# Kernel tuning notes

Hardware: AMD Instinct MI355X
Metric: run time of the kernel (lower is better)

## Reference

```python
import jax, jax.numpy as jnp
import numpy as np

S = 7          # grid_size
B = 2          # num_boxes
C = 80         # num_classes
LC = 5.0       # lambda_coord
LN = 0.5       # lambda_noobj
BT = 8192      # batch
N = 32         # gt boxes per image (distinct cells)


def setup_inputs() -> dict:
    key = jax.random.key(0)
    kp, kc, ko, kw, kl = jax.random.split(key, 5)
    preds = jax.random.normal(kp, (BT, S, S, B * 5 + C), jnp.float32)
    # choose N distinct grid cells per image so scatter-set is deterministic
    cells = jnp.argsort(jax.random.uniform(kc, (BT, S * S)), axis=-1)[:, :N]
    gi = cells % S
    gj = cells // S
    off = jax.random.uniform(ko, (BT, N, 2), minval=0.05, maxval=0.95)
    cx = (gi.astype(jnp.float32) + off[..., 0]) / S
    cy = (gj.astype(jnp.float32) + off[..., 1]) / S
    wh = jax.random.uniform(kw, (BT, N, 2), minval=0.05, maxval=0.3)
    gt_boxes = jnp.stack([cx - 0.5 * wh[..., 0], cy - 0.5 * wh[..., 1],
                          cx + 0.5 * wh[..., 0], cy + 0.5 * wh[..., 1]], axis=-1)
    gt_labels = jax.random.randint(kl, (BT, N), 0, C)
    gt_valid = jnp.ones((BT, N), dtype=bool)
    return {"preds": preds, "gt_boxes": gt_boxes,
            "gt_labels": gt_labels, "gt_valid": gt_valid}


def reference(preds, gt_boxes, gt_labels, gt_valid):
    Bt = preds.shape[0]
    dt = preds.dtype
    pred_cls = preds[..., B * 5:]                              # [Bt,S,S,C]
    pb = preds[..., :B * 5].reshape(Bt, S, S, B, 5)            # [Bt,S,S,B,5]

    x1, y1, x2, y2 = (gt_boxes[..., i] for i in range(4))      # each [Bt,N]
    cx = (x1 + x2) * 0.5
    cy = (y1 + y2) * 0.5
    w = jnp.maximum(x2 - x1, 1e-6)
    h = jnp.maximum(y2 - y1, 1e-6)
    gi = jnp.clip(jnp.floor(cx * S), 0, S - 1).astype(jnp.int32)
    gj = jnp.clip(jnp.floor(cy * S), 0, S - 1).astype(jnp.int32)

    bidx = jnp.arange(Bt, dtype=jnp.int32)[:, None]
    cell = pb[bidx, gj, gi]                                    # [Bt,N,B,5]

    # decode predicted boxes for the matched cell
    px = (jax.nn.sigmoid(cell[..., 0]) + gi[..., None].astype(dt)) / S
    py = (jax.nn.sigmoid(cell[..., 1]) + gj[..., None].astype(dt)) / S
    pw = cell[..., 2] ** 2
    ph = cell[..., 3] ** 2
    px1 = px - 0.5 * pw; py1 = py - 0.5 * ph
    px2 = px + 0.5 * pw; py2 = py + 0.5 * ph

    # IoU of B predicted boxes vs the gt box, vectorized over [Bt,N]
    gx1 = x1[..., None]; gy1 = y1[..., None]
    gx2 = x2[..., None]; gy2 = y2[..., None]
    iw = jnp.clip(jnp.minimum(px2, gx2) - jnp.maximum(px1, gx1), 0.0)
    ih = jnp.clip(jnp.minimum(py2, gy2) - jnp.maximum(py1, gy1), 0.0)
    inter = iw * ih
    area_p = (px2 - px1) * (py2 - py1)
    area_g = ((x2 - x1) * (y2 - y1))[..., None]
    ious = inter / (area_p + area_g - inter + 1e-6)            # [Bt,N,B]

    best = jnp.argmax(ious, axis=-1)                           # [Bt,N]
    iou_best = jax.lax.stop_gradient(
        jnp.take_along_axis(ious, best[..., None], axis=-1)[..., 0])

    # scatter target assignment (distinct cells -> deterministic set)
    flat_pb = Bt * S * S * B
    idx = ((bidx * S + gj) * S + gi) * B + best.astype(jnp.int32)
    idx = jnp.where(gt_valid, idx, flat_pb)                    # OOB -> dropped
    obj = jnp.zeros(flat_pb, bool).at[idx].set(True, mode='drop').reshape(Bt, S, S, B)
    conf_t = jnp.zeros(flat_pb, dt).at[idx].set(iou_best, mode='drop').reshape(Bt, S, S, B)
    tgt = jnp.stack([cx * S - gi.astype(dt), cy * S - gj.astype(dt),
                     jnp.sqrt(w), jnp.sqrt(h)], axis=-1)       # [Bt,N,4]
    coord_t = jnp.zeros((flat_pb, 4), dt).at[idx].set(tgt, mode='drop').reshape(Bt, S, S, B, 4)
    flat_c = Bt * S * S * C
    cidx = ((bidx * S + gj) * S + gi) * C + gt_labels.astype(jnp.int32)
    cidx = jnp.where(gt_valid, cidx, flat_c)
    cls_t = jnp.zeros(flat_c, dt).at[cidx].set(1.0, mode='drop').reshape(Bt, S, S, C)

    # masked MSE reductions
    pm = obj.astype(dt)
    nm = 1.0 - pm
    cm = obj.any(axis=-1).astype(dt)
    n_pos = jnp.maximum(pm.sum(), 1.0)
    n_neg = jnp.maximum(nm.sum(), 1.0)
    n_cell = jnp.maximum(cm.sum(), 1.0)

    sx = jax.nn.sigmoid(pb[..., 0])
    sy = jax.nn.sigmoid(pb[..., 1])
    so = jax.nn.sigmoid(pb[..., 4])
    loss_x = (pm * (sx - coord_t[..., 0]) ** 2).sum()
    loss_y = (pm * (sy - coord_t[..., 1]) ** 2).sum()
    loss_w = (pm * (pb[..., 2] - coord_t[..., 2]) ** 2).sum()
    loss_h = (pm * (pb[..., 3] - coord_t[..., 3]) ** 2).sum()
    loss_coord = LC * (loss_x + loss_y + loss_w + loss_h) / n_pos
    loss_obj = (pm * (so - conf_t) ** 2).sum() / n_pos
    loss_noobj = LN * (nm * (so - conf_t) ** 2).sum() / n_neg
    sp = jax.nn.softmax(pred_cls, axis=-1)
    loss_cls = (cm * ((sp - cls_t) ** 2).sum(axis=-1)).sum() / n_cell
    return loss_coord + loss_obj + loss_noobj + loss_cls
```

## Files before the change

### kernel.cpp

```cpp
#include <hip/hip_runtime.h>

#define S7 7
#define NCH 90
#define NCELL 49
#define NGT 32
#define IMG_FLOATS (NCELL * NCH)
#define IMG_F2     (IMG_FLOATS / 2)

__device__ __forceinline__ float sigm(float x) { return 1.0f / (1.0f + __expf(-x)); }

__global__ __launch_bounds__(256) void yolo_fused(
    const float*  __restrict__ preds,
    const float4* __restrict__ gt_boxes,
    const int*    __restrict__ gt_labels,
    float* __restrict__ ws,
    float c_coord, float c_obj, float c_noobj, float c_cls)
{
    __shared__ float s_img[IMG_FLOATS];
    __shared__ float s_red[4];

    const int t = threadIdx.x;
    const int b = blockIdx.x;
    const int g = t >> 3, u = t & 7;

    const int n = b * NGT + g;
    float4 gb = gt_boxes[n];
    int lab = gt_labels[n];

    const float2* img2 = (const float2*)(preds + (size_t)b * IMG_FLOATS);
    float2* s2 = (float2*)s_img;
    float2 v[9];
    #pragma unroll
    for (int k = 0; k < 9; ++k) {
        int idx = t + k * 256;
        if (idx < IMG_F2) v[k] = img2[idx];
    }
    #pragma unroll
    for (int k = 0; k < 9; ++k) {
        int idx = t + k * 256;
        if (idx < IMG_F2) s2[idx] = v[k];
    }

    float x1 = gb.x, y1 = gb.y, x2 = gb.z, y2 = gb.w;
    float cx = (x1 + x2) * 0.5f, cy = (y1 + y2) * 0.5f;
    float gif = fminf(fmaxf(floorf(cx * 7.f), 0.f), 6.f);
    float gjf = fminf(fmaxf(floorf(cy * 7.f), 0.f), 6.f);
    int cell = (int)gjf * S7 + (int)gif;

    __syncthreads();

    float part = 0.f;

    if (t < 2 * NCELL) {
        float so = sigm(s_img[(t >> 1) * NCH + 4 + 5 * (t & 1)]);
        part += c_noobj * so * so;
    }

    const float2* row2 = s2 + cell * (NCH / 2);
    float s = 0.f, q = 0.f, el = 0.f;
    {
        #pragma unroll
        for (int k = 0; k < 5; ++k) {
            float2 cv = row2[5 + 5 * u + k];
            float e0 = __expf(cv.x);
            float e1 = __expf(cv.y);
            int cid = 10 * u + 2 * k;
            s += e0 + e1;
            q = fmaf(e0, e0, q);
            q = fmaf(e1, e1, q);
            el = (cid     == lab) ? e0 : el;
            el = (cid + 1 == lab) ? e1 : el;
        }
        #pragma unroll
        for (int off = 1; off <= 4; off <<= 1) {
            s  += __shfl_xor(s,  off, 64);
            q  += __shfl_xor(q,  off, 64);
            el += __shfl_xor(el, off, 64);
        }
    }

    if (u == 0) {
        float inv = 1.f / s;
        part += c_cls * fmaf(q * inv, inv, fmaf(-2.f * el, inv, 1.f));

        float2 b0 = row2[0], b1 = row2[1], b2 = row2[2], b3 = row2[3], b4 = row2[4];
        float c[10] = {b0.x, b0.y, b1.x, b1.y, b2.x, b2.y, b3.x, b3.y, b4.x, b4.y};
        float w = fmaxf(x2 - x1, 1e-6f), h = fmaxf(y2 - y1, 1e-6f);
        float ag = (x2 - x1) * (y2 - y1);
        const float inv7 = 0.14285714285714285f;
        float iou[2];
        #pragma unroll
        for (int bb = 0; bb < 2; ++bb) {
            float px = (sigm(c[bb * 5 + 0]) + gif) * inv7;
            float py = (sigm(c[bb * 5 + 1]) + gjf) * inv7;
            float pw = c[bb * 5 + 2] * c[bb * 5 + 2];
            float ph = c[bb * 5 + 3] * c[bb * 5 + 3];
            float px1 = px - 0.5f * pw, px2 = px + 0.5f * pw;
            float py1 = py - 0.5f * ph, py2 = py + 0.5f * ph;
            float iw = fmaxf(fminf(px2, x2) - fmaxf(px1, x1), 0.f);
            float ih = fmaxf(fminf(py2, y2) - fmaxf(py1, y1), 0.f);
            float inter = iw * ih;
            float ap = (px2 - px1) * (py2 - py1);
            iou[bb] = inter / (ap + ag - inter + 1e-6f);
        }
        int best = (iou[1] > iou[0]) ? 1 : 0;
        float ioub = iou[best];
        float soB  = sigm(c[best * 5 + 4]);
        part += c_obj * (soB - ioub) * (soB - ioub);
        part -= c_noobj * soB * soB;
        float tx = cx * 7.f - gif, ty = cy * 7.f - gjf;
        float sx = sigm(c[best * 5 + 0]), sy = sigm(c[best * 5 + 1]);
        float dx = sx - tx, dy = sy - ty;
        float dw = c[best * 5 + 2] - sqrtf(w), dh = c[best * 5 + 3] - sqrtf(h);
        part += c_coord * (dx * dx + dy * dy + dw * dw + dh * dh);
    }

    #pragma unroll
    for (int off = 32; off >= 1; off >>= 1) part += __shfl_xor(part, off, 64);
    if ((t & 63) == 0) s_red[t >> 6] = part;
    __syncthreads();
    if (t == 0) ws[b] = s_red[0] + s_red[1] + s_red[2] + s_red[3];
}

__global__ __launch_bounds__(256) void yolo_reduce(const float* __restrict__ ws,
                                                   float* __restrict__ out, int n) {
    float v = 0.f;
    for (int i = threadIdx.x; i < n; i += 256) v += ws[i];
    #pragma unroll
    for (int off = 32; off >= 1; off >>= 1) v += __shfl_xor(v, off, 64);
    __shared__ float r[4];
    if ((threadIdx.x & 63) == 0) r[threadIdx.x >> 6] = v;
    __syncthreads();
    if (threadIdx.x == 0) out[0] = r[0] + r[1] + r[2] + r[3];
}

extern "C" void kernel_launch(void* const* d_in, const int* in_sizes, int n_in,
                              void* d_out, int out_size, void* d_ws, size_t ws_size,
                              hipStream_t stream)
{
    const float*  preds     = (const float*)d_in[0];
    const float4* gt_boxes  = (const float4*)d_in[1];
    const int*    gt_labels = (const int*)d_in[2];
    int Bt = in_sizes[0] / IMG_FLOATS;

    float n_pos = (float)Bt * NGT;
    float n_neg = (float)Bt * (2 * NCELL - NGT);
    float c_coord = 5.0f / n_pos;
    float c_obj   = 1.0f / n_pos;
    float c_noobj = 0.5f / n_neg;
    float c_cls   = 1.0f / n_pos;

    float* ws = (float*)d_ws;
    yolo_fused<<<dim3(Bt), dim3(256), 0, stream>>>(preds, gt_boxes, gt_labels, ws,
                                                   c_coord, c_obj, c_noobj, c_cls);
    yolo_reduce<<<dim3(1), dim3(256), 0, stream>>>(ws, (float*)d_out, Bt);
}
```

Baseline: 218.2 us.

## Make fused YOLO loss kernel persistent with double-buffered LDS prefetch

Launches at most 2048 blocks that loop over images in grid-stride order. The next image's predictions and gt data are loaded into registers while the current image is processed from one of two LDS buffers. This aims to hide global load latency and cut per-block launch and sync overhead, and the final reduction now covers fewer partials. The doubled LDS footprint and extra registers lower occupancy, which can offset the overlap.

```diff
diff --git a/kernel.cpp b/kernel.cpp
--- a/kernel.cpp
+++ b/kernel.cpp
@@ -6,6 +6,8 @@
 #define NGT 32
 #define IMG_FLOATS (NCELL * NCH)
 #define IMG_F2     (IMG_FLOATS / 2)
+#define LDS_F2     2208
+#define MAXBLK 2048
 
 __device__ __forceinline__ float sigm(float x) { return 1.0f / (1.0f + __expf(-x)); }
 
@@ -14,112 +16,129 @@
     const float4* __restrict__ gt_boxes,
     const int*    __restrict__ gt_labels,
     float* __restrict__ ws,
-    float c_coord, float c_obj, float c_noobj, float c_cls)
+    float c_coord, float c_obj, float c_noobj, float c_cls, int Bt)
 {
-    __shared__ float s_img[IMG_FLOATS];
-    __shared__ float s_red[4];
+    __shared__ float2 s_buf[2][LDS_F2];
+    __shared__ float  s_red[4];
 
     const int t = threadIdx.x;
-    const int b = blockIdx.x;
     const int g = t >> 3, u = t & 7;
+    const float inv7 = 0.14285714285714285f;
 
-    const int n = b * NGT + g;
-    float4 gb = gt_boxes[n];
-    int lab = gt_labels[n];
+    float part = 0.f;
+    int b = blockIdx.x;
+    int p = 0;
 
-    const float2* img2 = (const float2*)(preds + (size_t)b * IMG_FLOATS);
-    float2* s2 = (float2*)s_img;
-    float2 v[9];
-    #pragma unroll
-    for (int k = 0; k < 9; ++k) {
-        int idx = t + k * 256;
-        if (idx < IMG_F2) v[k] = img2[idx];
+    {
+        const float2* img2 = (const float2*)(preds + (size_t)b * IMG_FLOATS);
+        float2 v[9];
+        #pragma unroll
+        for (int k = 0; k < 9; ++k) { int i = t + k * 256; if (i < IMG_F2) v[k] = img2[i]; }
+        #pragma unroll
+        for (int k = 0; k < 9; ++k) { int i = t + k * 256; if (i < IMG_F2) s_buf[0][i] = v[k]; }
     }
-    #pragma unroll
-    for (int k = 0; k < 9; ++k) {
-        int idx = t + k * 256;
-        if (idx < IMG_F2) s2[idx] = v[k];
-    }
-
-    float x1 = gb.x, y1 = gb.y, x2 = gb.z, y2 = gb.w;
-    float cx = (x1 + x2) * 0.5f, cy = (y1 + y2) * 0.5f;
-    float gif = fminf(fmaxf(floorf(cx * 7.f), 0.f), 6.f);
-    float gjf = fminf(fmaxf(floorf(cy * 7.f), 0.f), 6.f);
-    int cell = (int)gjf * S7 + (int)gif;
-
+    float4 gb = gt_boxes[b * NGT + g];
+    int   lab = gt_labels[b * NGT + g];
     __syncthreads();
 
-    float part = 0.f;
+    while (true) {
+        const int bn = b + gridDim.x;
+        const bool more = bn < Bt;
 
-    if (t < 2 * NCELL) {
-        float so = sigm(s_img[(t >> 1) * NCH + 4 + 5 * (t & 1)]);
-        part += c_noobj * so * so;
-    }
+        float2 nv[9];
+        float4 ngb; int nlab;
+        if (more) {
+            const float2* img2 = (const float2*)(preds + (size_t)bn * IMG_FLOATS);
+            #pragma unroll
+            for (int k = 0; k < 9; ++k) { int i = t + k * 256; if (i < IMG_F2) nv[k] = img2[i]; }
+            ngb  = gt_boxes[bn * NGT + g];
+            nlab = gt_labels[bn * NGT + g];
+        }
 
-    const float2* row2 = s2 + cell * (NCH / 2);
-    float s = 0.f, q = 0.f, el = 0.f;
-    {
+        const float*  buff = (const float*)s_buf[p];
+        {
+            if (t < 2 * NCELL) {
+                float so = sigm(buff[(t >> 1) * NCH + 4 + 5 * (t & 1)]);
+                part += c_noobj * so * so;
+            }
+
+            float x1 = gb.x, y1 = gb.y, x2 = gb.z, y2 = gb.w;
+            float cx = (x1 + x2) * 0.5f, cy = (y1 + y2) * 0.5f;
+            float gif = fminf(fmaxf(floorf(cx * 7.f), 0.f), 6.f);
+            float gjf = fminf(fmaxf(floorf(cy * 7.f), 0.f), 6.f);
+            int cell = (int)gjf * S7 + (int)gif;
+            const float2* row2 = s_buf[p] + cell * (NCH / 2);
+
+            float s = 0.f, q = 0.f, el = 0.f;
+            #pragma unroll
+            for (int k = 0; k < 5; ++k) {
+                float2 cv = row2[5 + 5 * u + k];
+                float e0 = __expf(cv.x);
+                float e1 = __expf(cv.y);
+                int cid = 10 * u + 2 * k;
+                s += e0 + e1;
+                q = fmaf(e0, e0, q);
+                q = fmaf(e1, e1, q);
+                el = (cid     == lab) ? e0 : el;
+                el = (cid + 1 == lab) ? e1 : el;
+            }
+            #pragma unroll
+            for (int off = 1; off <= 4; off <<= 1) {
+                s  += __shfl_xor(s,  off, 64);
+                q  += __shfl_xor(q,  off, 64);
+                el += __shfl_xor(el, off, 64);
+            }
+
+            if (u == 0) {
+                float inv = 1.f / s;
+                part += c_cls * fmaf(q * inv, inv, fmaf(-2.f * el, inv, 1.f));
+
+                float2 b0 = row2[0], b1 = row2[1], b2 = row2[2], b3 = row2[3], b4 = row2[4];
+                float c[10] = {b0.x, b0.y, b1.x, b1.y, b2.x, b2.y, b3.x, b3.y, b4.x, b4.y};
+                float w = fmaxf(x2 - x1, 1e-6f), h = fmaxf(y2 - y1, 1e-6f);
+                float ag = (x2 - x1) * (y2 - y1);
+                float iou[2];
+                #pragma unroll
+                for (int bb = 0; bb < 2; ++bb) {
+                    float px = (sigm(c[bb * 5 + 0]) + gif) * inv7;
+                    float py = (sigm(c[bb * 5 + 1]) + gjf) * inv7;
+                    float pw = c[bb * 5 + 2] * c[bb * 5 + 2];
+                    float ph = c[bb * 5 + 3] * c[bb * 5 + 3];
+                    float px1 = px - 0.5f * pw, px2 = px + 0.5f * pw;
+                    float py1 = py - 0.5f * ph, py2 = py + 0.5f * ph;
+                    float iw = fmaxf(fminf(px2, x2) - fmaxf(px1, x1), 0.f);
+                    float ih = fmaxf(fminf(py2, y2) - fmaxf(py1, y1), 0.f);
+                    float inter = iw * ih;
+                    float ap = (px2 - px1) * (py2 - py1);
+                    iou[bb] = inter / (ap + ag - inter + 1e-6f);
+                }
+                int best = (iou[1] > iou[0]) ? 1 : 0;
+                float ioub = iou[best];
+                float soB  = sigm(c[best * 5 + 4]);
+                part += c_obj * (soB - ioub) * (soB - ioub);
+                part -= c_noobj * soB * soB;
+                float tx = cx * 7.f - gif, ty = cy * 7.f - gjf;
+                float sx = sigm(c[best * 5 + 0]), sy = sigm(c[best * 5 + 1]);
+                float dx = sx - tx, dy = sy - ty;
+                float dw = c[best * 5 + 2] - sqrtf(w), dh = c[best * 5 + 3] - sqrtf(h);
+                part += c_coord * (dx * dx + dy * dy + dw * dw + dh * dh);
+            }
+        }
+
+        if (!more) break;
+
         #pragma unroll
-        for (int k = 0; k < 5; ++k) {
-            float2 cv = row2[5 + 5 * u + k];
-            float e0 = __expf(cv.x);
-            float e1 = __expf(cv.y);
-            int cid = 10 * u + 2 * k;
-            s += e0 + e1;
-            q = fmaf(e0, e0, q);
-            q = fmaf(e1, e1, q);
-            el = (cid     == lab) ? e0 : el;
-            el = (cid + 1 == lab) ? e1 : el;
-        }
-        #pragma unroll
-        for (int off = 1; off <= 4; off <<= 1) {
-            s  += __shfl_xor(s,  off, 64);
-            q  += __shfl_xor(q,  off, 64);
-            el += __shfl_xor(el, off, 64);
-        }
-    }
-
-    if (u == 0) {
-        float inv = 1.f / s;
-        part += c_cls * fmaf(q * inv, inv, fmaf(-2.f * el, inv, 1.f));
-
-        float2 b0 = row2[0], b1 = row2[1], b2 = row2[2], b3 = row2[3], b4 = row2[4];
-        float c[10] = {b0.x, b0.y, b1.x, b1.y, b2.x, b2.y, b3.x, b3.y, b4.x, b4.y};
-        float w = fmaxf(x2 - x1, 1e-6f), h = fmaxf(y2 - y1, 1e-6f);
-        float ag = (x2 - x1) * (y2 - y1);
-        const float inv7 = 0.14285714285714285f;
-        float iou[2];
-        #pragma unroll
-        for (int bb = 0; bb < 2; ++bb) {
-            float px = (sigm(c[bb * 5 + 0]) + gif) * inv7;
-            float py = (sigm(c[bb * 5 + 1]) + gjf) * inv7;
-            float pw = c[bb * 5 + 2] * c[bb * 5 + 2];
-            float ph = c[bb * 5 + 3] * c[bb * 5 + 3];
-            float px1 = px - 0.5f * pw, px2 = px + 0.5f * pw;
-            float py1 = py - 0.5f * ph, py2 = py + 0.5f * ph;
-            float iw = fmaxf(fminf(px2, x2) - fmaxf(px1, x1), 0.f);
-            float ih = fmaxf(fminf(py2, y2) - fmaxf(py1, y1), 0.f);
-            float inter = iw * ih;
-            float ap = (px2 - px1) * (py2 - py1);
-            iou[bb] = inter / (ap + ag - inter + 1e-6f);
-        }
-        int best = (iou[1] > iou[0]) ? 1 : 0;
-        float ioub = iou[best];
-        float soB  = sigm(c[best * 5 + 4]);
-        part += c_obj * (soB - ioub) * (soB - ioub);
-        part -= c_noobj * soB * soB;
-        float tx = cx * 7.f - gif, ty = cy * 7.f - gjf;
-        float sx = sigm(c[best * 5 + 0]), sy = sigm(c[best * 5 + 1]);
-        float dx = sx - tx, dy = sy - ty;
-        float dw = c[best * 5 + 2] - sqrtf(w), dh = c[best * 5 + 3] - sqrtf(h);
-        part += c_coord * (dx * dx + dy * dy + dw * dw + dh * dh);
+        for (int k = 0; k < 9; ++k) { int i = t + k * 256; if (i < IMG_F2) s_buf[p ^ 1][i] = nv[k]; }
+        gb = ngb; lab = nlab;
+        __syncthreads();
+        p ^= 1; b = bn;
     }
 
     #pragma unroll
     for (int off = 32; off >= 1; off >>= 1) part += __shfl_xor(part, off, 64);
     if ((t & 63) == 0) s_red[t >> 6] = part;
     __syncthreads();
-    if (t == 0) ws[b] = s_red[0] + s_red[1] + s_red[2] + s_red[3];
+    if (t == 0) ws[blockIdx.x] = s_red[0] + s_red[1] + s_red[2] + s_red[3];
 }
 
 __global__ __launch_bounds__(256) void yolo_reduce(const float* __restrict__ ws,
@@ -150,8 +169,9 @@
     float c_noobj = 0.5f / n_neg;
     float c_cls   = 1.0f / n_pos;
 
+    int nblk = (Bt < MAXBLK) ? Bt : MAXBLK;
     float* ws = (float*)d_ws;
-    yolo_fused<<<dim3(Bt), dim3(256), 0, stream>>>(preds, gt_boxes, gt_labels, ws,
-                                                   c_coord, c_obj, c_noobj, c_cls);
-    yolo_reduce<<<dim3(1), dim3(256), 0, stream>>>(ws, (float*)d_out, Bt);
+    yolo_fused<<<dim3(nblk), dim3(256), 0, stream>>>(preds, gt_boxes, gt_labels, ws,
+                                                     c_coord, c_obj, c_noobj, c_cls, Bt);
+    yolo_reduce<<<dim3(1), dim3(256), 0, stream>>>(ws, (float*)d_out, nblk);
 }
```

Measured after the change: 216.3 us. About the same (-0.9%).
